# Optimization experiments

Measured on AMD Instinct MI355X. Metric: run time of the kernel, lower is better.

Reference implementation:

```python
import jax, jax.numpy as jnp
from jax import lax
import numpy as np


def conv4d(x, w, b, pad):
    """4D conv (stride 1) as a sum of 3D convs over the first-spatial-dim kernel taps.
    x: [B, Cin, T, D, H, W]; w: [Cout, Cin, Kt, Kd, Kh, Kw]; same pad on all dims."""
    B, Cin, T, D, H, W = x.shape
    Cout, _, Kt = w.shape[:3]
    xp = jnp.pad(x, ((0, 0), (0, 0), (pad, pad), (0, 0), (0, 0), (0, 0)))
    Tout = T + 2 * pad - Kt + 1
    acc = None
    for k in range(Kt):  # loop over kernel taps (<=3), not data dims
        xs = xp[:, :, k:k + Tout]                      # [B,Cin,Tout,D,H,W]
        xs = xs.transpose(0, 2, 1, 3, 4, 5).reshape(B * Tout, Cin, D, H, W)
        y = lax.conv_general_dilated(
            xs, w[:, :, k], (1, 1, 1), [(pad, pad)] * 3,
            dimension_numbers=('NCDHW', 'OIDHW', 'NCDHW'))
        acc = y if acc is None else acc + y
    Do, Ho, Wo = acc.shape[2:]
    out = acc.reshape(B, Tout, Cout, Do, Ho, Wo).transpose(0, 2, 1, 3, 4, 5)
    return out + b[None, :, None, None, None, None]


def tconv4d_k2s2(x, w, b):
    """4D transposed conv, kernel=2, stride=2, pad=0 (non-overlapping blocks).
    x: [B,Cin,T,D,H,W]; w: [Cin,Cout,2,2,2,2] (PyTorch ConvTranspose layout)."""
    B, Cin, T, D, H, W = x.shape
    Cout = w.shape[1]
    y = jnp.einsum('bcijkl,copqrs->boipjqkrls', x, w)
    y = y.reshape(B, Cout, 2 * T, 2 * D, 2 * H, 2 * W)
    return y + b[None, :, None, None, None, None]


def setup_inputs() -> dict:
    key = jax.random.key(0)
    ks = jax.random.split(key, 10)
    Cin, Cout = 64, 32
    x1 = jax.random.normal(ks[0], (2, Cin, 8, 8, 8, 8), dtype=jnp.float32)
    x2 = jax.random.normal(ks[1], (2, Cin // 2, 16, 16, 16, 16), dtype=jnp.float32)
    def w(k, shape, fan_in):
        return jax.random.normal(k, shape, dtype=jnp.float32) / np.float32(np.sqrt(fan_in))
    up_w = w(ks[2], (Cin, Cin // 2, 2, 2, 2, 2), Cin * 16)
    up_b = w(ks[3], (Cin // 2,), Cin * 16)
    w1 = w(ks[4], (Cout, Cin, 3, 3, 3, 3), Cin * 81)
    b1 = w(ks[5], (Cout,), Cin * 81)
    w2 = w(ks[6], (Cout, Cout, 3, 3, 3, 3), Cout * 81)
    b2 = w(ks[7], (Cout,), Cout * 81)
    w3 = w(ks[8], (Cout, Cin, 1, 1, 1, 1), Cin)
    b3 = w(ks[9], (Cout,), Cin)
    return {'x1': x1, 'x2': x2, 'up_w': up_w, 'up_b': up_b,
            'w1': w1, 'b1': b1, 'w2': w2, 'b2': b2, 'w3': w3, 'b3': b3}


def reference(x1, x2, up_w, up_b, w1, b1, w2, b2, w3, b3):
    x1u = tconv4d_k2s2(x1, up_w, up_b)              # [B, Cin//2, 16,16,16,16]
    xc = jnp.concatenate([x2, x1u], axis=1)          # [B, Cin, 16,16,16,16]
    Y = jax.nn.relu(conv4d(xc, w1, b1, 1))
    Y = conv4d(Y, w2, b2, 1)
    sc = conv4d(xc, w3, b3, 0)                       # 1x1 residual projection
    return jax.nn.relu(Y + sc)
```

## Files before the change

kernel.cpp:

```cpp
#include <hip/hip_runtime.h>

typedef unsigned short u16;
typedef __attribute__((ext_vector_type(8))) short short8;
typedef __attribute__((ext_vector_type(4))) float f32x4;

#define XCB_OFF  0
#define Y1B_OFF  8388608
#define W1P_OFF  12582912
#define W2P_OFF  12748800
#define W3P_OFF  12831744
#define UPWP_OFF 12833792
#define ZPAD_OFF 12866560

__device__ __forceinline__ u16 f2bf(float v) {
    unsigned u = __builtin_bit_cast(unsigned, v);
    u += 0x7FFFu + ((u >> 16) & 1u);
    return (u16)(u >> 16);
}

__device__ __forceinline__ f32x4 MFMA(short8 a, short8 b, f32x4 c) {
    return __builtin_amdgcn_mfma_f32_16x16x32_bf16(a, b, c, 0, 0, 0);
}

typedef const __attribute__((address_space(1))) u16 gas_u16;
typedef __attribute__((address_space(3))) u16 las_u16;
__device__ __forceinline__ void gload16(const u16* g, u16* l) {
    __builtin_amdgcn_global_load_lds((gas_u16*)g, (las_u16*)l, 16, 0, 0);
}

__global__ __launch_bounds__(256) void setup(const float* __restrict__ w1,
                                             const float* __restrict__ w2,
                                             const float* __restrict__ w3,
                                             const float* __restrict__ upw,
                                             const float* __restrict__ x2,
                                             u16* __restrict__ ws) {
    __shared__ u16 lds[256 * 40];
    int bid = blockIdx.x;
    int tid = threadIdx.x;
    if (bid == 0 && tid < 64) ws[ZPAD_OFF + tid] = 0;
    if (bid < 512) {
        int b = bid >> 8;
        int pos_base = (bid & 255) * 256;
        u16* xcb = ws + XCB_OFF;
        #pragma unroll
        for (int c = 0; c < 32; ++c) {
            lds[tid * 40 + c] = f2bf(x2[((b * 32 + c) << 16) + pos_base + tid]);
        }
        __syncthreads();
        #pragma unroll
        for (int k = 0; k < 4; ++k) {
            int f = k * 256 + tid;
            int u = f & 3, pos = f >> 2;
            uint4 v = *(const uint4*)(lds + pos * 40 + u * 8);
            *(uint4*)(xcb + (size_t)((b << 16) + pos_base + pos) * 64 + u * 8) = v;
        }
    } else {
        int idx = (bid - 512) * 256 + tid;
        if (idx < 165888) {
            int j = idx & 7, lane = (idx >> 3) & 63, rest = idx >> 9;
            int half = rest & 1, chunk = (rest >> 1) & 1, tap = rest >> 2;
            int co = half * 16 + (lane & 15), ci = chunk * 32 + (lane >> 4) * 8 + j;
            ws[W1P_OFF + idx] = f2bf(w1[(co * 64 + ci) * 81 + tap]);
        } else if (idx < 165888 + 82944) {
            int i2 = idx - 165888;
            int j = i2 & 7, lane = (i2 >> 3) & 63, rest = i2 >> 9;
            int half = rest & 1, tap = rest >> 1;
            int co = half * 16 + (lane & 15), ci = (lane >> 4) * 8 + j;
            ws[W2P_OFF + i2] = f2bf(w2[(co * 32 + ci) * 81 + tap]);
        } else if (idx < 165888 + 82944 + 2048) {
            int i3 = idx - (165888 + 82944);
            int j = i3 & 7, lane = (i3 >> 3) & 63, rest = i3 >> 9;
            int half = rest & 1, chunk = rest >> 1;
            int co = half * 16 + (lane & 15), ci = chunk * 32 + (lane >> 4) * 8 + j;
            ws[W3P_OFF + i3] = f2bf(w3[co * 64 + ci]);
        } else if (idx < 250880 + 32768) {
            int i4 = idx - 250880;
            int j = i4 & 7, lane = (i4 >> 3) & 63, rest = i4 >> 9;
            int half = rest & 1, chunk = (rest >> 1) & 1, tap = rest >> 2;
            int co = half * 16 + (lane & 15), ci = chunk * 32 + (lane >> 4) * 8 + j;
            ws[UPWP_OFF + i4] = f2bf(upw[(ci * 32 + co) * 16 + tap]);
        }
    }
}

__global__ __launch_bounds__(256) void xc_up_mfma(const float* __restrict__ x1,
                                                  const u16* __restrict__ upwp,
                                                  const float* __restrict__ up_b,
                                                  u16* __restrict__ xcb) {
    __shared__ u16 lds[64 * 72];
    int tid = threadIdx.x;
    int wv = tid >> 6, lane = tid & 63;
    int q = lane >> 4, m = lane & 15;
    int bid = blockIdx.x;
    int tp = bid & 1, j = (bid >> 1) & 63, b = bid >> 7;
    int pos_base = j * 64;

    #pragma unroll
    for (int g = 0; g < 16; ++g) {
        int c = g * 4 + wv;
        lds[lane * 72 + c] = f2bf(x1[((b * 64 + c) << 12) + pos_base + lane]);
    }
    __syncthreads();

    const short8* wv8 = (const short8*)upwp;
    float4 bi0 = ((const float4*)up_b)[q];
    float4 bi1 = ((const float4*)up_b)[4 + q];
    int it = j >> 3, id = j & 7;

    for (int tt = 0; tt < 2; ++tt) {
        int tap = tp * 8 + wv * 2 + tt;
        f32x4 acc[4][2];
        #pragma unroll
        for (int g = 0; g < 4; ++g) {
            acc[g][0] = (f32x4){bi0.x, bi0.y, bi0.z, bi0.w};
            acc[g][1] = (f32x4){bi1.x, bi1.y, bi1.z, bi1.w};
        }
        #pragma unroll
        for (int chunk = 0; chunk < 2; ++chunk) {
            short8 a0 = wv8[((tap * 2 + chunk) * 2 + 0) * 64 + lane];
            short8 a1 = wv8[((tap * 2 + chunk) * 2 + 1) * 64 + lane];
            #pragma unroll
            for (int g = 0; g < 4; ++g) {
                short8 bf = *(const short8*)(lds + (g * 16 + m) * 72 + chunk * 32 + q * 8);
                acc[g][0] = MFMA(a0, bf, acc[g][0]);
                acc[g][1] = MFMA(a1, bf, acc[g][1]);
            }
        }
        int pt = tap >> 3, pd = (tap >> 2) & 1, ph = (tap >> 1) & 1, pw = tap & 1;
        int oT = 2 * it + pt, oD = 2 * id + pd, oW = 2 * (m & 7) + pw;
        #pragma unroll
        for (int g = 0; g < 4; ++g) {
            int ih = g * 2 + (m >> 3);
            int opos = oT * 4096 + oD * 256 + (2 * ih + ph) * 16 + oW;
            u16* op = xcb + (size_t)((b << 16) + opos) * 64 + 32 + q * 4;
            #pragma unroll
            for (int half = 0; half < 2; ++half) {
                f32x4 v = acc[g][half];
                uint2 o;
                o.x = (unsigned)f2bf(v.x) | ((unsigned)f2bf(v.y) << 16);
                o.y = (unsigned)f2bf(v.z) | ((unsigned)f2bf(v.w) << 16);
                *(uint2*)(op + half * 16) = o;
            }
        }
    }
}

__global__ __launch_bounds__(256, 2) void conv1_mfma(const u16* __restrict__ xcb,
                                                     const u16* __restrict__ w1p,
                                                     const float* __restrict__ b1,
                                                     const u16* __restrict__ zpad,
                                                     u16* __restrict__ y1b) {
    __shared__ __attribute__((aligned(16))) u16 lds[27648];
    int tid = threadIdx.x;
    int lane = tid & 63, wv = tid >> 6;
    int q = lane >> 4, m = lane & 15;
    int c = wv & 1, rg = wv >> 1;
    int bid = blockIdx.x;
    int xcd = bid & 7;
    int b = xcd >> 2, tq = xcd & 3;
    int loc = bid >> 3;
    int hB = loc & 1;
    int d = (loc >> 1) & 15;
    int tl = (loc >> 5) & 3;
    int t = tq * 4 + tl;
    int h0 = hB * 8;
    int rot = (bid * 5) % 9;

    int gofs[6], lofs[6];
    bool st[6], inr[6];
    #pragma unroll
    for (int k = 0; k < 6; ++k) {
        int ui = tid + k * 256;
        int hh = ui / 144, rem = ui - hh * 144;
        int p = rem >> 3, w = rem & 7;
        int u_src = w ^ (p & 7);
        int gh = h0 - 1 + hh, gw = p - 1;
        st[k] = ui < 1440;
        inr[k] = st[k] && ((unsigned)gh < 16u) && ((unsigned)gw < 16u);
        gofs[k] = (gh * 16 + gw) * 64 + u_src * 8;
        lofs[k] = ui * 8;
    }

    f32x4 acc[4][2];
    if (c == 0) {
        float4 bi0 = ((const float4*)b1)[q];
        float4 bi1 = ((const float4*)b1)[4 + q];
        #pragma unroll
        for (int i = 0; i < 4; ++i) {
            acc[i][0] = (f32x4){bi0.x, bi0.y, bi0.z, bi0.w};
            acc[i][1] = (f32x4){bi1.x, bi1.y, bi1.z, bi1.w};
        }
    } else {
        #pragma unroll
        for (int i = 0; i < 4; ++i) {
            acc[i][0] = (f32x4){0.f, 0.f, 0.f, 0.f};
            acc[i][1] = (f32x4){0.f, 0.f, 0.f, 0.f};
        }
    }
    const short8* w1v = (const short8*)w1p;

    auto issue_plane = [&](int ktd, int bb) {
        int kt = ktd / 3, kd = ktd - kt * 3;
        int tt = t + kt - 1, dd = d + kd - 1;
        bool pv = ((unsigned)tt < 16u) && ((unsigned)dd < 16u);
        const u16* src = xcb + (size_t)(((b * 16 + tt) * 16 + dd)) * 16384;
        #pragma unroll
        for (int k = 0; k < 6; ++k) {
            if (st[k]) {
                const u16* g = (pv && inr[k]) ? (src + gofs[k]) : zpad;
                gload16(g, lds + bb * 13824 + lofs[k]);
            }
        }
    };

    issue_plane(rot, 0);
    for (int s = 0; s < 9; ++s) {
        int ktd = rot + s; if (ktd >= 9) ktd -= 9;
        int kt = ktd / 3, kd = ktd - kt * 3;
        __syncthreads();
        short8 W[3][3][2];
        #pragma unroll
        for (int kw = 0; kw < 3; ++kw)
            #pragma unroll
            for (int kh = 0; kh < 3; ++kh) {
                int tap = ((kt * 3 + kd) * 3 + kh) * 3 + kw;
                W[kw][kh][0] = w1v[((tap * 2 + c) * 2 + 0) * 64 + lane];
                W[kw][kh][1] = w1v[((tap * 2 + c) * 2 + 1) * 64 + lane];
            }
        __builtin_amdgcn_sched_barrier(0);
        if (s < 8) {
            int nk = ktd + 1; if (nk >= 9) nk -= 9;
            issue_plane(nk, (s + 1) & 1);
        }
        __builtin_amdgcn_sched_barrier(0);
        const u16* L = lds + (s & 1) * 13824;
        __builtin_amdgcn_s_setprio(1);
        #pragma unroll
        for (int kw = 0; kw < 3; ++kw) {
            int p = kw + m, pm = p & 7;
            int bo = p * 64 + ((((c << 2) | q) ^ pm) << 3);
            short8 R[6];
            #pragma unroll
            for (int r = 0; r < 6; ++r)
                R[r] = *(const short8*)(L + (rg * 4 + r) * 1152 + bo);
            #pragma unroll
            for (int kh = 0; kh < 3; ++kh) {
                #pragma unroll
                for (int i = 0; i < 4; ++i) {
                    acc[i][0] = MFMA(W[kw][kh][0], R[i + kh], acc[i][0]);
                    acc[i][1] = MFMA(W[kw][kh][1], R[i + kh], acc[i][1]);
                }
            }
        }
        __builtin_amdgcn_s_setprio(0);
    }

    __syncthreads();
    f32x4* buf = (f32x4*)lds;
    if (c == 1) {
        #pragma unroll
        for (int i = 0; i < 4; ++i)
            #pragma unroll
            for (int half = 0; half < 2; ++half)
                buf[((rg * 4 + i) * 2 + half) * 64 + lane] = acc[i][half];
    }
    __syncthreads();
    if (c == 0) {
        int obase = ((b * 16 + t) * 16 + d) * 256 + (h0 + rg * 4) * 16 + m;
        #pragma unroll
        for (int i = 0; i < 4; ++i) {
            int pos = obase + i * 16;
            #pragma unroll
            for (int half = 0; half < 2; ++half) {
                f32x4 v = acc[i][half];
                f32x4 w = buf[((rg * 4 + i) * 2 + half) * 64 + lane];
                v.x += w.x; v.y += w.y; v.z += w.z; v.w += w.w;
                unsigned r0 = f2bf(fmaxf(v.x, 0.f)), r1 = f2bf(fmaxf(v.y, 0.f));
                unsigned r2 = f2bf(fmaxf(v.z, 0.f)), r3 = f2bf(fmaxf(v.w, 0.f));
                uint2 o;
                o.x = r0 | (r1 << 16);
                o.y = r2 | (r3 << 16);
                *(uint2*)(y1b + (size_t)pos * 32 + half * 16 + q * 4) = o;
            }
        }
    }
}

__global__ __launch_bounds__(256, 2) void conv2_mfma(const u16* __restrict__ y1b,
                                                     const u16* __restrict__ xcb,
                                                     const u16* __restrict__ w2p,
                                                     const u16* __restrict__ w3p,
                                                     const float* __restrict__ b2,
                                                     const float* __restrict__ b3,
                                                     const u16* __restrict__ zpad,
                                                     float* __restrict__ out) {
    __shared__ __attribute__((aligned(16))) u16 lds[20736];
    int tid = threadIdx.x;
    int lane = tid & 63, wv = tid >> 6;
    int q = lane >> 4, m = lane & 15;
    int rg = wv;
    int bid = blockIdx.x;
    int xcd = bid & 7;
    int b = xcd >> 2, tq = xcd & 3;
    int loc = bid >> 3;
    int d = loc & 15;
    int tl = (loc >> 4) & 3;
    int t = tq * 4 + tl;
    int rot = (bid * 5) % 9;

    int gofs[6], lofs[6];
    bool st[6], inr[6];
    #pragma unroll
    for (int k = 0; k < 6; ++k) {
        int ui = tid + k * 256;
        int hh = ui / 72, rem = ui - hh * 72;
        int p = rem >> 2, w = rem & 3;
        int u_src = w ^ (p & 3);
        int gh = hh - 1, gw = p - 1;
        st[k] = ui < 1296;
        inr[k] = st[k] && ((unsigned)gh < 16u) && ((unsigned)gw < 16u);
        gofs[k] = (gh * 16 + gw) * 32 + u_src * 8;
        lofs[k] = ui * 8;
    }

    f32x4 acc[4][2];
    #pragma unroll
    for (int hf = 0; hf < 2; ++hf) {
        float4 p0 = ((const float4*)b2)[hf * 4 + q];
        float4 s0 = ((const float4*)b3)[hf * 4 + q];
        #pragma unroll
        for (int i = 0; i < 4; ++i)
            acc[i][hf] = (f32x4){p0.x + s0.x, p0.y + s0.y, p0.z + s0.z, p0.w + s0.w};
    }
    const short8* w2v = (const short8*)w2p;

    auto issue_plane = [&](int ktd, int bb) {
        int kt = ktd / 3, kd = ktd - kt * 3;
        int tt = t + kt - 1, dd = d + kd - 1;
        bool pv = ((unsigned)tt < 16u) && ((unsigned)dd < 16u);
        const u16* src = y1b + (size_t)(((b * 16 + tt) * 16 + dd)) * 8192;
        #pragma unroll
        for (int k = 0; k < 6; ++k) {
            if (st[k]) {
                const u16* g = (pv && inr[k]) ? (src + gofs[k]) : zpad;
                gload16(g, lds + bb * 10368 + lofs[k]);
            }
        }
    };

    issue_plane(rot, 0);
    for (int s = 0; s < 9; ++s) {
        int ktd = rot + s; if (ktd >= 9) ktd -= 9;
        __syncthreads();
        short8 W[3][3][2];
        #pragma unroll
        for (int kw = 0; kw < 3; ++kw)
            #pragma unroll
            for (int kh = 0; kh < 3; ++kh) {
                int tap = (ktd * 3 + kh) * 3 + kw;
                W[kw][kh][0] = w2v[(tap * 2 + 0) * 64 + lane];
                W[kw][kh][1] = w2v[(tap * 2 + 1) * 64 + lane];
            }
        __builtin_amdgcn_sched_barrier(0);
        if (s < 8) {
            int nk = ktd + 1; if (nk >= 9) nk -= 9;
            issue_plane(nk, (s + 1) & 1);
        }
        __builtin_amdgcn_sched_barrier(0);
        const u16* L = lds + (s & 1) * 10368;
        __builtin_amdgcn_s_setprio(1);
        #pragma unroll
        for (int kw = 0; kw < 3; ++kw) {
            int p = kw + m, pm = p & 3;
            int bo = p * 32 + ((q ^ pm) << 3);
            short8 R[6];
            #pragma unroll
            for (int r = 0; r < 6; ++r)
                R[r] = *(const short8*)(L + (rg * 4 + r) * 576 + bo);
            #pragma unroll
            for (int kh = 0; kh < 3; ++kh) {
                #pragma unroll
                for (int i = 0; i < 4; ++i) {
                    acc[i][0] = MFMA(W[kw][kh][0], R[i + kh], acc[i][0]);
                    acc[i][1] = MFMA(W[kw][kh][1], R[i + kh], acc[i][1]);
                }
            }
        }
        __builtin_amdgcn_s_setprio(0);
    }

    const short8* w3v = (const short8*)w3p;
    int lpos0 = (t * 16 + d) * 256 + (rg * 4) * 16 + m;
    int gpos0 = (b << 16) + lpos0;
    #pragma unroll
    for (int chunk = 0; chunk < 2; ++chunk) {
        short8 a0 = w3v[(chunk * 2 + 0) * 64 + lane];
        short8 a1 = w3v[(chunk * 2 + 1) * 64 + lane];
        #pragma unroll
        for (int i = 0; i < 4; ++i) {
            short8 bf = *(const short8*)(xcb + (size_t)(gpos0 + i * 16) * 64 + ((chunk << 2) | q) * 8);
            acc[i][0] = MFMA(a0, bf, acc[i][0]);
            acc[i][1] = MFMA(a1, bf, acc[i][1]);
        }
    }

    #pragma unroll
    for (int i = 0; i < 4; ++i) {
        int lpos = lpos0 + i * 16;
        #pragma unroll
        for (int hf = 0; hf < 2; ++hf) {
            f32x4 v = acc[i][hf];
            int co = hf * 16 + q * 4;
            float* op = out + (((size_t)(b * 32 + co)) << 16) + lpos;
            op[0ull << 16] = fmaxf(v.x, 0.f);
            op[1ull << 16] = fmaxf(v.y, 0.f);
            op[2ull << 16] = fmaxf(v.z, 0.f);
            op[3ull << 16] = fmaxf(v.w, 0.f);
        }
    }
}

extern "C" void kernel_launch(void* const* d_in, const int* in_sizes, int n_in,
                              void* d_out, int out_size, void* d_ws, size_t ws_size,
                              hipStream_t stream) {
    const float* x1   = (const float*)d_in[0];
    const float* x2   = (const float*)d_in[1];
    const float* up_w = (const float*)d_in[2];
    const float* up_b = (const float*)d_in[3];
    const float* w1   = (const float*)d_in[4];
    const float* b1   = (const float*)d_in[5];
    const float* w2   = (const float*)d_in[6];
    const float* b2   = (const float*)d_in[7];
    const float* w3   = (const float*)d_in[8];
    const float* b3   = (const float*)d_in[9];
    u16* ws  = (u16*)d_ws;
    float* out = (float*)d_out;

    setup<<<1620, 256, 0, stream>>>(w1, w2, w3, up_w, x2, ws);
    xc_up_mfma<<<256, 256, 0, stream>>>(x1, ws + UPWP_OFF, up_b, ws + XCB_OFF);
    conv1_mfma<<<1024, 256, 0, stream>>>(ws + XCB_OFF, ws + W1P_OFF, b1,
                                         ws + ZPAD_OFF, ws + Y1B_OFF);
    conv2_mfma<<<512, 256, 0, stream>>>(ws + Y1B_OFF, ws + XCB_OFF, ws + W2P_OFF,
                                        ws + W3P_OFF, b2, b3, ws + ZPAD_OFF, out);
}
```

Baseline: 155.9 us.

## Re-split conv warps by output-channel half with 8-row tiles instead of 4-row tiles

In both conv kernels each wave now owns one 16-channel half of the outputs across 8 h-rows, where before it owned both halves across 4 rows. Each wave loads half as many weight fragments but 10 LDS input rows instead of 6, so per-wave weight register traffic and global weight loads drop while LDS reads rise. The conv1 cross-wave reduction and the epilogues are reindexed to match. The goal is to shift work toward better reuse of the input rows across the kh taps, at the cost of more row reads and different register pressure.

```diff
diff --git a/kernel.cpp b/kernel.cpp
--- a/kernel.cpp
+++ b/kernel.cpp
@@ -154,7 +154,7 @@
     int tid = threadIdx.x;
     int lane = tid & 63, wv = tid >> 6;
     int q = lane >> 4, m = lane & 15;
-    int c = wv & 1, rg = wv >> 1;
+    int c = wv & 1, hf = wv >> 1;
     int bid = blockIdx.x;
     int xcd = bid & 7;
     int b = xcd >> 2, tq = xcd & 3;
@@ -181,21 +181,16 @@
         lofs[k] = ui * 8;
     }
 
-    f32x4 acc[4][2];
+    f32x4 acc[8];
     if (c == 0) {
-        float4 bi0 = ((const float4*)b1)[q];
-        float4 bi1 = ((const float4*)b1)[4 + q];
-        #pragma unroll
-        for (int i = 0; i < 4; ++i) {
-            acc[i][0] = (f32x4){bi0.x, bi0.y, bi0.z, bi0.w};
-            acc[i][1] = (f32x4){bi1.x, bi1.y, bi1.z, bi1.w};
-        }
+        float4 bi = ((const float4*)b1)[hf * 4 + q];
+        #pragma unroll
+        for (int i = 0; i < 8; ++i)
+            acc[i] = (f32x4){bi.x, bi.y, bi.z, bi.w};
     } else {
         #pragma unroll
-        for (int i = 0; i < 4; ++i) {
-            acc[i][0] = (f32x4){0.f, 0.f, 0.f, 0.f};
-            acc[i][1] = (f32x4){0.f, 0.f, 0.f, 0.f};
-        }
+        for (int i = 0; i < 8; ++i)
+            acc[i] = (f32x4){0.f, 0.f, 0.f, 0.f};
     }
     const short8* w1v = (const short8*)w1p;
 
@@ -218,14 +213,13 @@
         int ktd = rot + s; if (ktd >= 9) ktd -= 9;
         int kt = ktd / 3, kd = ktd - kt * 3;
         __syncthreads();
-        short8 W[3][3][2];
+        short8 W[3][3];
         #pragma unroll
         for (int kw = 0; kw < 3; ++kw)
             #pragma unroll
             for (int kh = 0; kh < 3; ++kh) {
                 int tap = ((kt * 3 + kd) * 3 + kh) * 3 + kw;
-                W[kw][kh][0] = w1v[((tap * 2 + c) * 2 + 0) * 64 + lane];
-                W[kw][kh][1] = w1v[((tap * 2 + c) * 2 + 1) * 64 + lane];
+                W[kw][kh] = w1v[((tap * 2 + c) * 2 + hf) * 64 + lane];
             }
         __builtin_amdgcn_sched_barrier(0);
         if (s < 8) {
@@ -239,17 +233,15 @@
         for (int kw = 0; kw < 3; ++kw) {
             int p = kw + m, pm = p & 7;
             int bo = p * 64 + ((((c << 2) | q) ^ pm) << 3);
-            short8 R[6];
-            #pragma unroll
-            for (int r = 0; r < 6; ++r)
-                R[r] = *(const short8*)(L + (rg * 4 + r) * 1152 + bo);
+            short8 R[10];
+            #pragma unroll
+            for (int r = 0; r < 10; ++r)
+                R[r] = *(const short8*)(L + r * 1152 + bo);
             #pragma unroll
             for (int kh = 0; kh < 3; ++kh) {
                 #pragma unroll
-                for (int i = 0; i < 4; ++i) {
-                    acc[i][0] = MFMA(W[kw][kh][0], R[i + kh], acc[i][0]);
-                    acc[i][1] = MFMA(W[kw][kh][1], R[i + kh], acc[i][1]);
-                }
+                for (int i = 0; i < 8; ++i)
+                    acc[i] = MFMA(W[kw][kh], R[i + kh], acc[i]);
             }
         }
         __builtin_amdgcn_s_setprio(0);
@@ -259,29 +251,24 @@
     f32x4* buf = (f32x4*)lds;
     if (c == 1) {
         #pragma unroll
-        for (int i = 0; i < 4; ++i)
-            #pragma unroll
-            for (int half = 0; half < 2; ++half)
-                buf[((rg * 4 + i) * 2 + half) * 64 + lane] = acc[i][half];
+        for (int i = 0; i < 8; ++i)
+            buf[(hf * 8 + i) * 64 + lane] = acc[i];
     }
     __syncthreads();
     if (c == 0) {
-        int obase = ((b * 16 + t) * 16 + d) * 256 + (h0 + rg * 4) * 16 + m;
-        #pragma unroll
-        for (int i = 0; i < 4; ++i) {
+        int obase = ((b * 16 + t) * 16 + d) * 256 + h0 * 16 + m;
+        #pragma unroll
+        for (int i = 0; i < 8; ++i) {
             int pos = obase + i * 16;
-            #pragma unroll
-            for (int half = 0; half < 2; ++half) {
-                f32x4 v = acc[i][half];
-                f32x4 w = buf[((rg * 4 + i) * 2 + half) * 64 + lane];
-                v.x += w.x; v.y += w.y; v.z += w.z; v.w += w.w;
-                unsigned r0 = f2bf(fmaxf(v.x, 0.f)), r1 = f2bf(fmaxf(v.y, 0.f));
-                unsigned r2 = f2bf(fmaxf(v.z, 0.f)), r3 = f2bf(fmaxf(v.w, 0.f));
-                uint2 o;
-                o.x = r0 | (r1 << 16);
-                o.y = r2 | (r3 << 16);
-                *(uint2*)(y1b + (size_t)pos * 32 + half * 16 + q * 4) = o;
-            }
+            f32x4 v = acc[i];
+            f32x4 w = buf[(hf * 8 + i) * 64 + lane];
+            v.x += w.x; v.y += w.y; v.z += w.z; v.w += w.w;
+            unsigned r0 = f2bf(fmaxf(v.x, 0.f)), r1 = f2bf(fmaxf(v.y, 0.f));
+            unsigned r2 = f2bf(fmaxf(v.z, 0.f)), r3 = f2bf(fmaxf(v.w, 0.f));
+            uint2 o;
+            o.x = r0 | (r1 << 16);
+            o.y = r2 | (r3 << 16);
+            *(uint2*)(y1b + (size_t)pos * 32 + hf * 16 + q * 4) = o;
         }
     }
 }
@@ -298,7 +285,7 @@
     int tid = threadIdx.x;
     int lane = tid & 63, wv = tid >> 6;
     int q = lane >> 4, m = lane & 15;
-    int rg = wv;
+    int hf = wv & 1, rh = wv >> 1;
     int bid = blockIdx.x;
     int xcd = bid & 7;
     int b = xcd >> 2, tq = xcd & 3;
@@ -323,14 +310,13 @@
         lofs[k] = ui * 8;
     }
 
-    f32x4 acc[4][2];
-    #pragma unroll
-    for (int hf = 0; hf < 2; ++hf) {
+    f32x4 acc[8];
+    {
         float4 p0 = ((const float4*)b2)[hf * 4 + q];
         float4 s0 = ((const float4*)b3)[hf * 4 + q];
         #pragma unroll
-        for (int i = 0; i < 4; ++i)
-            acc[i][hf] = (f32x4){p0.x + s0.x, p0.y + s0.y, p0.z + s0.z, p0.w + s0.w};
+        for (int i = 0; i < 8; ++i)
+            acc[i] = (f32x4){p0.x + s0.x, p0.y + s0.y, p0.z + s0.z, p0.w + s0.w};
     }
     const short8* w2v = (const short8*)w2p;
 
@@ -352,14 +338,13 @@
     for (int s = 0; s < 9; ++s) {
         int ktd = rot + s; if (ktd >= 9) ktd -= 9;
         __syncthreads();
-        short8 W[3][3][2];
+        short8 W[3][3];
         #pragma unroll
         for (int kw = 0; kw < 3; ++kw)
             #pragma unroll
             for (int kh = 0; kh < 3; ++kh) {
                 int tap = (ktd * 3 + kh) * 3 + kw;
-                W[kw][kh][0] = w2v[(tap * 2 + 0) * 64 + lane];
-                W[kw][kh][1] = w2v[(tap * 2 + 1) * 64 + lane];
+                W[kw][kh] = w2v[(tap * 2 + hf) * 64 + lane];
             }
         __builtin_amdgcn_sched_barrier(0);
         if (s < 8) {
@@ -373,50 +358,43 @@
         for (int kw = 0; kw < 3; ++kw) {
             int p = kw + m, pm = p & 3;
             int bo = p * 32 + ((q ^ pm) << 3);
-            short8 R[6];
-            #pragma unroll
-            for (int r = 0; r < 6; ++r)
-                R[r] = *(const short8*)(L + (rg * 4 + r) * 576 + bo);
+            short8 R[10];
+            #pragma unroll
+            for (int r = 0; r < 10; ++r)
+                R[r] = *(const short8*)(L + (rh * 8 + r) * 576 + bo);
             #pragma unroll
             for (int kh = 0; kh < 3; ++kh) {
                 #pragma unroll
-                for (int i = 0; i < 4; ++i) {
-                    acc[i][0] = MFMA(W[kw][kh][0], R[i + kh], acc[i][0]);
-                    acc[i][1] = MFMA(W[kw][kh][1], R[i + kh], acc[i][1]);
-                }
+                for (int i = 0; i < 8; ++i)
+                    acc[i] = MFMA(W[kw][kh], R[i + kh], acc[i]);
             }
         }
         __builtin_amdgcn_s_setprio(0);
     }
 
     const short8* w3v = (const short8*)w3p;
-    int lpos0 = (t * 16 + d) * 256 + (rg * 4) * 16 + m;
+    int lpos0 = (t * 16 + d) * 256 + (rh * 8) * 16 + m;
     int gpos0 = (b << 16) + lpos0;
     #pragma unroll
     for (int chunk = 0; chunk < 2; ++chunk) {
-        short8 a0 = w3v[(chunk * 2 + 0) * 64 + lane];
-        short8 a1 = w3v[(chunk * 2 + 1) * 64 + lane];
-        #pragma unroll
-        for (int i = 0; i < 4; ++i) {
+        short8 a = w3v[(chunk * 2 + hf) * 64 + lane];
+        #pragma unroll
+        for (int i = 0; i < 8; ++i) {
             short8 bf = *(const short8*)(xcb + (size_t)(gpos0 + i * 16) * 64 + ((chunk << 2) | q) * 8);
-            acc[i][0] = MFMA(a0, bf, acc[i][0]);
-            acc[i][1] = MFMA(a1, bf, acc[i][1]);
+            acc[i] = MFMA(a, bf, acc[i]);
         }
     }
 
     #pragma unroll
-    for (int i = 0; i < 4; ++i) {
+    for (int i = 0; i < 8; ++i) {
         int lpos = lpos0 + i * 16;
-        #pragma unroll
-        for (int hf = 0; hf < 2; ++hf) {
-            f32x4 v = acc[i][hf];
-            int co = hf * 16 + q * 4;
-            float* op = out + (((size_t)(b * 32 + co)) << 16) + lpos;
-            op[0ull << 16] = fmaxf(v.x, 0.f);
-            op[1ull << 16] = fmaxf(v.y, 0.f);
-            op[2ull << 16] = fmaxf(v.z, 0.f);
-            op[3ull << 16] = fmaxf(v.w, 0.f);
-        }
+        f32x4 v = acc[i];
+        int co = hf * 16 + q * 4;
+        float* op = out + (((size_t)(b * 32 + co)) << 16) + lpos;
+        op[0ull << 16] = fmaxf(v.x, 0.f);
+        op[1ull << 16] = fmaxf(v.y, 0.f);
+        op[2ull << 16] = fmaxf(v.z, 0.f);
+        op[3ull << 16] = fmaxf(v.w, 0.f);
     }
 }
 
```

New measurement: 155.3 us (median of 2 runs). Within noise of the previous version (-0.4%).
